# Performance work log

Hardware: AMD Instinct MI355X
Metric: run time of the kernel (lower is better)

Reference implementation:

```python
import jax, jax.numpy as jnp
import numpy as np

N_NODES = 100000
N_EDGES = 3200000
F_IN = 256
HIDDEN = 16
N_CLASSES = 32


def setup_inputs() -> dict:
    key = jax.random.key(0)
    ks = jax.random.split(key, 9)
    x = jax.random.normal(ks[0], (N_NODES, F_IN), dtype=jnp.float32)
    edge_index = jax.random.randint(ks[1], (2, N_EDGES), 0, N_NODES)
    edge_attr = jax.random.uniform(ks[2], (N_EDGES, 1), dtype=jnp.float32)
    s1 = 1.0 / np.sqrt(F_IN)
    W1 = jax.random.normal(ks[3], (2, F_IN, HIDDEN), dtype=jnp.float32) * s1
    root1 = jax.random.normal(ks[4], (F_IN, HIDDEN), dtype=jnp.float32) * s1
    bias1 = jnp.zeros((HIDDEN,), dtype=jnp.float32)
    s2 = 1.0 / np.sqrt(HIDDEN)
    W2 = jax.random.normal(ks[5], (2, HIDDEN, N_CLASSES), dtype=jnp.float32) * s2
    root2 = jax.random.normal(ks[6], (HIDDEN, N_CLASSES), dtype=jnp.float32) * s2
    bias2 = jnp.zeros((N_CLASSES,), dtype=jnp.float32)
    return {"x": x, "edge_attr": edge_attr, "W1": W1, "root1": root1,
            "bias1": bias1, "W2": W2, "root2": root2, "bias2": bias2,
            "edge_index": edge_index}


def spline_conv(x, src, dst, u, W, root, bias):
    """SplineConv, dim=1, kernel_size=2, degree=1, open spline, aggr='mean'.

    With K=2 and degree-1 open splines, v = u*(K-1) = u, so the B-spline basis
    per edge is simply ((1-u), u) over kernel weights W[0], W[1].
    """
    n = x.shape[0]
    # Node-level GEMMs once (cheaper than per-edge F_IN-dim gathers): [2, N, out]
    xs = jnp.einsum('nf,kfo->kno', x, W)
    # Per-edge basis-weighted message from source nodes: [E, out]
    msg = (1.0 - u)[:, None] * xs[0, src] + u[:, None] * xs[1, src]
    agg = jax.ops.segment_sum(msg, dst, num_segments=n)
    cnt = jax.ops.segment_sum(jnp.ones((dst.shape[0],), x.dtype), dst,
                              num_segments=n)
    return agg / jnp.maximum(cnt, 1.0)[:, None] + x @ root + bias


def reference(x, edge_attr, W1, root1, bias1, W2, root2, bias2, edge_index):
    src, dst = edge_index[0], edge_index[1]
    u = jnp.clip(edge_attr[:, 0], 0.0, 1.0)  # pseudo coords in [0, 1]
    # dropout with training=False is identity (eval-mode reference)
    h = jax.nn.elu(spline_conv(x, src, dst, u, W1, root1, bias1))
    out = spline_conv(h, src, dst, u, W2, root2, bias2)
    return jax.nn.log_softmax(out, axis=1)
```

## Files before the change

kernel.cpp:

```cpp
#include <hip/hip_runtime.h>
#include <hip/hip_fp16.h>
#include <math.h>

#define NN 100000
#define NE 3200000
#define FIN 256
#define HID 16
#define NC 32
#define NBUK 782
#define CAP 5120
#define SC_BLOCKS 250
#define SC_TILE 12800
#define SC_EPT 13
#define SK 20

typedef __attribute__((ext_vector_type(8))) short short8;
typedef __attribute__((ext_vector_type(4))) float f32x4;
typedef union { uint4 u; short8 s; } U8;

__global__ __launch_bounds__(256) void k_prepB(
    const float* __restrict__ W1, const float* __restrict__ root1,
    uint4* __restrict__ Bpk)
{
    int idx = blockIdx.x * 256 + threadIdx.x;
    if (idx >= 1536) return;
    int c = idx & 15, kc = (idx >> 4) & 31, t = idx >> 9;
    unsigned hi[8], lo[8];
    #pragma unroll
    for (int e = 0; e < 8; ++e) {
        int k = kc * 8 + e;
        float v;
        if (t == 0)      v = W1[k * 16 + c];
        else if (t == 1) v = W1[FIN * 16 + k * 16 + c];
        else             v = root1[k * 16 + c];
        unsigned u = __float_as_uint(v);
        unsigned h = u & 0xFFFF0000u;
        float lf = v - __uint_as_float(h);
        hi[e] = h;
        lo[e] = __float_as_uint(lf) & 0xFFFF0000u;
    }
    uint4 H, L;
    H.x = (hi[0] >> 16) | hi[1];  H.y = (hi[2] >> 16) | hi[3];
    H.z = (hi[4] >> 16) | hi[5];  H.w = (hi[6] >> 16) | hi[7];
    L.x = (lo[0] >> 16) | lo[1];  L.y = (lo[2] >> 16) | lo[3];
    L.z = (lo[4] >> 16) | lo[5];  L.w = (lo[6] >> 16) | lo[7];
    Bpk[(size_t)idx * 2]     = H;
    Bpk[(size_t)idx * 2 + 1] = L;
}

__global__ __launch_bounds__(256) void k_gemm1(
    const float* __restrict__ x, const uint4* __restrict__ Bpk,
    const float* __restrict__ bias1,
    __half2* __restrict__ xs1p, __half2* __restrict__ r1h)
{
    int wid = (blockIdx.x << 2) + (threadIdx.x >> 6);
    if (wid >= NN / 16) return;
    int lane = threadIdx.x & 63;
    int c = lane & 15, kcl = lane >> 4;
    int n0 = wid * 16;

    const float* xr = x + (size_t)(n0 + c) * FIN + kcl * 8;
    f32x4 acc0 = {0.f, 0.f, 0.f, 0.f};
    f32x4 acc1 = {0.f, 0.f, 0.f, 0.f};
    f32x4 acc2 = {0.f, 0.f, 0.f, 0.f};

    #define PACK(f0, f1, HO, LO) {                                     \
        unsigned u0 = __float_as_uint(f0), u1 = __float_as_uint(f1);   \
        unsigned h0 = u0 & 0xFFFF0000u, h1 = u1 & 0xFFFF0000u;         \
        HO = (h0 >> 16) | h1;                                          \
        float l0 = (f0) - __uint_as_float(h0);                         \
        float l1 = (f1) - __uint_as_float(h1);                         \
        LO = (__float_as_uint(l0) >> 16) |                             \
             (__float_as_uint(l1) & 0xFFFF0000u); }

    #pragma unroll
    for (int s = 0; s < 8; ++s) {
        float4 a0 = *(const float4*)(xr + s * 32);
        float4 a1 = *(const float4*)(xr + s * 32 + 4);
        U8 ahi, alo;
        PACK(a0.x, a0.y, ahi.u.x, alo.u.x)
        PACK(a0.z, a0.w, ahi.u.y, alo.u.y)
        PACK(a1.x, a1.y, ahi.u.z, alo.u.z)
        PACK(a1.z, a1.w, ahi.u.w, alo.u.w)

        const uint4* bp = Bpk + ((size_t)((s * 4 + kcl) * 16 + c)) * 2;
        U8 bh0, bl0, bh1, bl1, bh2, bl2;
        bh0.u = bp[0];     bl0.u = bp[1];
        bh1.u = bp[1024];  bl1.u = bp[1025];
        bh2.u = bp[2048];  bl2.u = bp[2049];

        acc0 = __builtin_amdgcn_mfma_f32_16x16x32_bf16(ahi.s, bh0.s, acc0, 0, 0, 0);
        acc0 = __builtin_amdgcn_mfma_f32_16x16x32_bf16(alo.s, bh0.s, acc0, 0, 0, 0);
        acc0 = __builtin_amdgcn_mfma_f32_16x16x32_bf16(ahi.s, bl0.s, acc0, 0, 0, 0);
        acc1 = __builtin_amdgcn_mfma_f32_16x16x32_bf16(ahi.s, bh1.s, acc1, 0, 0, 0);
        acc1 = __builtin_amdgcn_mfma_f32_16x16x32_bf16(alo.s, bh1.s, acc1, 0, 0, 0);
        acc1 = __builtin_amdgcn_mfma_f32_16x16x32_bf16(ahi.s, bl1.s, acc1, 0, 0, 0);
        acc2 = __builtin_amdgcn_mfma_f32_16x16x32_bf16(ahi.s, bh2.s, acc2, 0, 0, 0);
        acc2 = __builtin_amdgcn_mfma_f32_16x16x32_bf16(alo.s, bh2.s, acc2, 0, 0, 0);
        acc2 = __builtin_amdgcn_mfma_f32_16x16x32_bf16(ahi.s, bl2.s, acc2, 0, 0, 0);
    }
    #undef PACK

    #pragma unroll
    for (int r = 0; r < 4; ++r) {
        int n = n0 + kcl * 4 + r;
        xs1p[(size_t)n * 16 + c] = __floats2half2_rn(acc0[r], acc1[r]);
    }
    float b = bias1[c];
    #pragma unroll
    for (int r = 0; r < 4; ++r) {
        int n = n0 + kcl * 4 + r;
        float v = acc2[r] + b;
        float vo = __shfl_xor(v, 1, 64);
        if (!(c & 1))
            r1h[(size_t)n * 8 + (c >> 1)] = __floats2half2_rn(v, vo);
    }
}

__global__ __launch_bounds__(1024) void k_binscatter(
    const int* __restrict__ ei, const float* __restrict__ ea,
    int* __restrict__ gcnt, uint2* __restrict__ rec)
{
    __shared__ int h[NBUK];
    int t = threadIdx.x;
    if (t < NBUK) h[t] = 0;
    __syncthreads();
    int e0 = blockIdx.x * SC_TILE;
    int   dl[SC_EPT];
    int   sl[SC_EPT];
    float ul[SC_EPT];
    #pragma unroll
    for (int k = 0; k < SC_EPT; ++k) {
        int i = t + k * 1024;
        if (i < SC_TILE) {
            dl[k] = ei[NE + e0 + i];
            sl[k] = ei[e0 + i];
            ul[k] = ea[e0 + i];
            atomicAdd(&h[dl[k] >> 7], 1);
        }
    }
    __syncthreads();
    if (t < NBUK) {
        int c = h[t];
        if (c) h[t] = t * CAP + atomicAdd(&gcnt[t], c);
    }
    __syncthreads();
    #pragma unroll
    for (int k = 0; k < SC_EPT; ++k) {
        int i = t + k * 1024;
        if (i < SC_TILE) {
            float u = fminf(fmaxf(ul[k], 0.f), 1.f);
            int pos = atomicAdd(&h[dl[k] >> 7], 1);
            uint2 r;
            r.x = (unsigned)sl[k] | ((unsigned)(dl[k] & 127) << 17);
            r.y = __float_as_uint(u);
            rec[pos] = r;
        }
    }
}

__global__ __launch_bounds__(256) void k_sort(
    const int* __restrict__ gcnt, uint2* __restrict__ rec,
    int* __restrict__ rstart, int* __restrict__ rend)
{
    __shared__ int cnt[128], cur[128], ss[128];
    int t = threadIdx.x;
    if (t < 128) cnt[t] = 0;
    __syncthreads();
    int start = blockIdx.x * CAP, m = gcnt[blockIdx.x];
    uint2 r[SK];
    int nr = 0;
    for (int i = start + t; i < start + m; i += 256) {
        uint2 v = rec[i];
        if (nr < SK) r[nr++] = v;
        atomicAdd(&cnt[(v.x >> 17) & 127], 1);
    }
    __syncthreads();
    if (t < 128) ss[t] = cnt[t];
    __syncthreads();
    for (int off = 1; off < 128; off <<= 1) {
        int a = (t < 128 && t >= off) ? ss[t - off] : 0;
        __syncthreads();
        if (t < 128) ss[t] += a;
        __syncthreads();
    }
    if (t < 128) {
        int excl = ss[t] - cnt[t];
        cur[t] = excl;
        int n = blockIdx.x * 128 + t;
        if (n < NN) {
            rstart[n] = start + excl;
            rend[n]   = start + excl + cnt[t];
        }
    }
    __syncthreads();
    for (int k = 0; k < nr; ++k) {
        int dl = (int)(r[k].x >> 17) & 127;
        int p = atomicAdd(&cur[dl], 1);
        rec[start + p] = r[k];
    }
}

__global__ __launch_bounds__(256) void k_agg1g2(
    const int* __restrict__ rstart, const int* __restrict__ rend,
    const uint2* __restrict__ rec, const uint2* __restrict__ xs,
    const __half2* __restrict__ r1h, __half2* __restrict__ hh2)
{
    int t = threadIdx.x;
    int nl = t >> 3, j = t & 7;
    int n = blockIdx.x * 32 + nl;
    int s = rstart[n], e = rend[n];
    int d = e - s;
    float a0 = 0.f, a1 = 0.f;

    #define ACC1(q, g) {                                            \
        float u = __uint_as_float((q).y);                           \
        float2 f0 = __half22float2(*(const __half2*)&(g).x);        \
        float2 f1 = __half22float2(*(const __half2*)&(g).y);        \
        a0 += (1.f - u) * f0.x + u * f0.y;                          \
        a1 += (1.f - u) * f1.x + u * f1.y; }

    int k = s;
    for (; k + 8 <= e; k += 8) {
        uint2 q[8], g[8];
        #pragma unroll
        for (int z = 0; z < 8; ++z) q[z] = rec[k + z];
        #pragma unroll
        for (int z = 0; z < 8; ++z) g[z] = xs[(size_t)(q[z].x & 0x1FFFF) * 8 + j];
        #pragma unroll
        for (int z = 0; z < 8; ++z) { ACC1(q[z], g[z]) }
    }
    for (; k < e; ++k) {
        uint2 q = rec[k];
        uint2 g = xs[(size_t)(q.x & 0x1FFFF) * 8 + j];
        ACC1(q, g)
    }
    #undef ACC1

    float inv = 1.f / fmaxf((float)d, 1.f);
    float2 rr = __half22float2(r1h[(size_t)n * 8 + j]);
    float v0 = a0 * inv + rr.x;
    float v1 = a1 * inv + rr.y;
    v0 = v0 > 0.f ? v0 : expm1f(v0);
    v1 = v1 > 0.f ? v1 : expm1f(v1);
    hh2[(size_t)n * 8 + j] = __floats2half2_rn(v0, v1);
}

__global__ __launch_bounds__(256) void k_agg2(
    const int* __restrict__ rstart, const int* __restrict__ rend,
    const uint2* __restrict__ rec, const uint2* __restrict__ hh,
    const float* __restrict__ W2, const float* __restrict__ root2,
    const float* __restrict__ bias2, float* __restrict__ out)
{
    __shared__ float wsm[1568];
    __shared__ float ssm[64 * 33];
    __shared__ float hv[64 * 18];
    int t = threadIdx.x;
    for (int i = t; i < 1568; i += 256)
        wsm[i] = (i < 1024) ? W2[i] : (i < 1536 ? root2[i - 1024] : bias2[i - 1536]);

    int nl = t >> 2, j = t & 3;
    int n = blockIdx.x * 64 + nl;
    bool valid = n < NN;
    int s = 0, e = 0;
    if (valid) { s = rstart[n]; e = rend[n]; }
    float s0[4] = {0.f, 0.f, 0.f, 0.f};
    float s1[4] = {0.f, 0.f, 0.f, 0.f};

    #define ACC2(q, g) {                                            \
        float u = __uint_as_float((q).y);                           \
        float w0 = 1.f - u;                                         \
        float2 f0 = __half22float2(*(const __half2*)&(g).x);        \
        float2 f1 = __half22float2(*(const __half2*)&(g).y);        \
        s0[0] += w0 * f0.x; s1[0] += u * f0.x;                      \
        s0[1] += w0 * f0.y; s1[1] += u * f0.y;                      \
        s0[2] += w0 * f1.x; s1[2] += u * f1.x;                      \
        s0[3] += w0 * f1.y; s1[3] += u * f1.y; }

    int k = s;
    for (; k + 8 <= e; k += 8) {
        uint2 q[8], g[8];
        #pragma unroll
        for (int z = 0; z < 8; ++z) q[z] = rec[k + z];
        #pragma unroll
        for (int z = 0; z < 8; ++z) g[z] = hh[(size_t)(q[z].x & 0x1FFFF) * 4 + j];
        #pragma unroll
        for (int z = 0; z < 8; ++z) { ACC2(q[z], g[z]) }
    }
    for (; k < e; ++k) {
        uint2 q = rec[k];
        uint2 g = hh[(size_t)(q.x & 0x1FFFF) * 4 + j];
        ACC2(q, g)
    }
    #undef ACC2

    float inv = 1.f / fmaxf((float)(e - s), 1.f);
    #pragma unroll
    for (int q2 = 0; q2 < 4; ++q2) {
        ssm[nl * 33 + 4 * j + q2] = s0[q2];
        ssm[nl * 33 + 16 + 4 * j + q2] = s1[q2];
    }
    if (valid) {
        uint2 gh = hh[(size_t)n * 4 + j];
        float2 h0 = __half22float2(*(const __half2*)&gh.x);
        float2 h1 = __half22float2(*(const __half2*)&gh.y);
        hv[nl * 18 + 4 * j]     = h0.x;
        hv[nl * 18 + 4 * j + 1] = h0.y;
        hv[nl * 18 + 4 * j + 2] = h1.x;
        hv[nl * 18 + 4 * j + 3] = h1.y;
    } else {
        hv[nl * 18 + 4 * j]     = 0.f;
        hv[nl * 18 + 4 * j + 1] = 0.f;
        hv[nl * 18 + 4 * j + 2] = 0.f;
        hv[nl * 18 + 4 * j + 3] = 0.f;
    }
    if (j == 0) hv[nl * 18 + 16] = inv;
    __syncthreads();

    float invn = hv[nl * 18 + 16];
    float v[8];
    #pragma unroll
    for (int cc = 0; cc < 8; ++cc) {
        int c = j * 8 + cc;
        float acc = wsm[1536 + c];
        float agg = 0.f;
        #pragma unroll
        for (int kk = 0; kk < 16; ++kk) {
            agg += ssm[nl * 33 + kk] * wsm[kk * 32 + c]
                 + ssm[nl * 33 + 16 + kk] * wsm[512 + kk * 32 + c];
            acc += hv[nl * 18 + kk] * wsm[1024 + kk * 32 + c];
        }
        v[cc] = acc + agg * invn;
    }

    float m = v[0];
    #pragma unroll
    for (int cc = 1; cc < 8; ++cc) m = fmaxf(m, v[cc]);
    #pragma unroll
    for (int off = 1; off < 4; off <<= 1)
        m = fmaxf(m, __shfl_xor(m, off, 4));
    float sm = 0.f;
    #pragma unroll
    for (int cc = 0; cc < 8; ++cc) sm += expf(v[cc] - m);
    #pragma unroll
    for (int off = 1; off < 4; off <<= 1)
        sm += __shfl_xor(sm, off, 4);
    float ls = m + logf(sm);
    if (valid) {
        float4* op = (float4*)(out + (size_t)n * 32 + j * 8);
        op[0] = make_float4(v[0] - ls, v[1] - ls, v[2] - ls, v[3] - ls);
        op[1] = make_float4(v[4] - ls, v[5] - ls, v[6] - ls, v[7] - ls);
    }
}

extern "C" void kernel_launch(void* const* d_in, const int* in_sizes, int n_in,
                              void* d_out, int out_size, void* d_ws, size_t ws_size,
                              hipStream_t stream)
{
    const float* x     = (const float*)d_in[0];
    const float* ea    = (const float*)d_in[1];
    const float* W1    = (const float*)d_in[2];
    const float* root1 = (const float*)d_in[3];
    const float* bias1 = (const float*)d_in[4];
    const float* W2    = (const float*)d_in[5];
    const float* root2 = (const float*)d_in[6];
    const float* bias2 = (const float*)d_in[7];
    const int*   ei    = (const int*)d_in[8];
    float* out = (float*)d_out;

    float* ws = (float*)d_ws;
    __half2* xs1p = (__half2*)ws;
    __half2* r1h  = (__half2*)(ws + (size_t)NN * 16);
    __half2* hh2  = (__half2*)(ws + (size_t)NN * 24);
    uint2*   rec  = (uint2*)(ws + (size_t)NN * 32);
    int*     iws  = (int*)(ws + (size_t)NN * 32 + (size_t)NBUK * CAP * 2);
    int* rstart = iws;
    int* rend   = iws + NN;
    int* gcnt   = iws + 2 * NN;
    uint4* Bpk = (uint4*)(ws + (size_t)NN * 24);

    hipMemsetAsync(gcnt, 0, NBUK * sizeof(int), stream);

    k_prepB<<<6, 256, 0, stream>>>(W1, root1, Bpk);
    k_gemm1<<<(NN / 16 + 3) / 4, 256, 0, stream>>>(x, Bpk, bias1, xs1p, r1h);
    k_binscatter<<<SC_BLOCKS, 1024, 0, stream>>>(ei, ea, gcnt, rec);
    k_sort<<<NBUK, 256, 0, stream>>>(gcnt, rec, rstart, rend);
    k_agg1g2<<<(NN * 8) / 256, 256, 0, stream>>>(rstart, rend, rec,
                                                 (const uint2*)xs1p, r1h, hh2);
    k_agg2<<<(NN + 63) / 64, 256, 0, stream>>>(rstart, rend, rec,
                                               (const uint2*)hh2,
                                               W2, root2, bias2, out);
}
```

Baseline: 382.4 us.

## Replace per-bucket sort with shared-memory atomic aggregation per destination bucket

Removes the k_sort pass and the rstart/rend CSR arrays. Each block now walks one 128-node destination bucket's unsorted records and accumulates messages into shared-memory float accumulators with LDS atomics, counting degrees the same way. This saves a full read/write pass over the edge records and one kernel launch. In exchange it adds heavy LDS atomic contention, and the per-node dense tail in layer 2 (32 outputs by 16 features) now runs on only 128 of 512 threads.

Measured after the change: 1.292 ms. 3.38x slower.

```diff
diff --git a/kernel.cpp b/kernel.cpp
--- a/kernel.cpp
+++ b/kernel.cpp
@@ -12,7 +12,6 @@
 #define SC_BLOCKS 250
 #define SC_TILE 12800
 #define SC_EPT 13
-#define SK 20
 
 typedef __attribute__((ext_vector_type(8))) short short8;
 typedef __attribute__((ext_vector_type(4))) float f32x4;
@@ -159,197 +158,155 @@
     }
 }
 
-__global__ __launch_bounds__(256) void k_sort(
-    const int* __restrict__ gcnt, uint2* __restrict__ rec,
-    int* __restrict__ rstart, int* __restrict__ rend)
-{
-    __shared__ int cnt[128], cur[128], ss[128];
+__global__ __launch_bounds__(512) void k_agg1b(
+    const int* __restrict__ gcnt, const uint2* __restrict__ rec,
+    const uint2* __restrict__ xs, const __half2* __restrict__ r1h,
+    __half2* __restrict__ hh2)
+{
+    __shared__ float acc[128 * 17];
+    __shared__ int cnt[128];
     int t = threadIdx.x;
+    #pragma unroll
+    for (int i = t; i < 128 * 17; i += 512) acc[i] = 0.f;
     if (t < 128) cnt[t] = 0;
     __syncthreads();
-    int start = blockIdx.x * CAP, m = gcnt[blockIdx.x];
-    uint2 r[SK];
-    int nr = 0;
-    for (int i = start + t; i < start + m; i += 256) {
-        uint2 v = rec[i];
-        if (nr < SK) r[nr++] = v;
-        atomicAdd(&cnt[(v.x >> 17) & 127], 1);
-    }
-    __syncthreads();
-    if (t < 128) ss[t] = cnt[t];
-    __syncthreads();
-    for (int off = 1; off < 128; off <<= 1) {
-        int a = (t < 128 && t >= off) ? ss[t - off] : 0;
-        __syncthreads();
-        if (t < 128) ss[t] += a;
-        __syncthreads();
-    }
+
+    int b = blockIdx.x;
+    int base = b * CAP, m = gcnt[b];
+    int rl = t >> 3, j = t & 7;
+
+    #define DO1(q, g) {                                                 \
+        int dl_ = ((q).x >> 17) & 127;                                  \
+        float u_ = __uint_as_float((q).y);                              \
+        float2 f0 = __half22float2(*(const __half2*)&(g).x);            \
+        float2 f1 = __half22float2(*(const __half2*)&(g).y);            \
+        atomicAdd(&acc[dl_ * 17 + 2 * j],     (1.f - u_) * f0.x + u_ * f0.y); \
+        atomicAdd(&acc[dl_ * 17 + 2 * j + 1], (1.f - u_) * f1.x + u_ * f1.y); \
+        if (j == 0) atomicAdd(&cnt[dl_], 1); }
+
+    int k = rl;
+    for (; k + 256 <= m; k += 256) {
+        uint2 q[4], g[4];
+        #pragma unroll
+        for (int z = 0; z < 4; ++z) q[z] = rec[base + k + 64 * z];
+        #pragma unroll
+        for (int z = 0; z < 4; ++z) g[z] = xs[(size_t)(q[z].x & 0x1FFFF) * 8 + j];
+        #pragma unroll
+        for (int z = 0; z < 4; ++z) { DO1(q[z], g[z]) }
+    }
+    for (; k < m; k += 64) {
+        uint2 q = rec[base + k];
+        uint2 g = xs[(size_t)(q.x & 0x1FFFF) * 8 + j];
+        DO1(q, g)
+    }
+    #undef DO1
+    __syncthreads();
+
     if (t < 128) {
-        int excl = ss[t] - cnt[t];
-        cur[t] = excl;
-        int n = blockIdx.x * 128 + t;
+        int n = b * 128 + t;
         if (n < NN) {
-            rstart[n] = start + excl;
-            rend[n]   = start + excl + cnt[t];
+            float inv = 1.f / fmaxf((float)cnt[t], 1.f);
+            __half2* hp = hh2 + (size_t)n * 8;
+            const __half2* rp = r1h + (size_t)n * 8;
+            #pragma unroll
+            for (int w = 0; w < 8; ++w) {
+                float2 rr = __half22float2(rp[w]);
+                float v0 = acc[t * 17 + 2 * w] * inv + rr.x;
+                float v1 = acc[t * 17 + 2 * w + 1] * inv + rr.y;
+                v0 = v0 > 0.f ? v0 : expm1f(v0);
+                v1 = v1 > 0.f ? v1 : expm1f(v1);
+                hp[w] = __floats2half2_rn(v0, v1);
+            }
         }
     }
-    __syncthreads();
-    for (int k = 0; k < nr; ++k) {
-        int dl = (int)(r[k].x >> 17) & 127;
-        int p = atomicAdd(&cur[dl], 1);
-        rec[start + p] = r[k];
-    }
-}
-
-__global__ __launch_bounds__(256) void k_agg1g2(
-    const int* __restrict__ rstart, const int* __restrict__ rend,
-    const uint2* __restrict__ rec, const uint2* __restrict__ xs,
-    const __half2* __restrict__ r1h, __half2* __restrict__ hh2)
-{
+}
+
+__global__ __launch_bounds__(512) void k_agg2b(
+    const int* __restrict__ gcnt, const uint2* __restrict__ rec,
+    const __half2* __restrict__ hh, const float* __restrict__ W2,
+    const float* __restrict__ root2, const float* __restrict__ bias2,
+    float* __restrict__ out)
+{
+    __shared__ float wsm[1568];
+    __shared__ float acc[128 * 33];
+    __shared__ int cnt[128];
     int t = threadIdx.x;
-    int nl = t >> 3, j = t & 7;
-    int n = blockIdx.x * 32 + nl;
-    int s = rstart[n], e = rend[n];
-    int d = e - s;
-    float a0 = 0.f, a1 = 0.f;
-
-    #define ACC1(q, g) {                                            \
-        float u = __uint_as_float((q).y);                           \
-        float2 f0 = __half22float2(*(const __half2*)&(g).x);        \
-        float2 f1 = __half22float2(*(const __half2*)&(g).y);        \
-        a0 += (1.f - u) * f0.x + u * f0.y;                          \
-        a1 += (1.f - u) * f1.x + u * f1.y; }
-
-    int k = s;
-    for (; k + 8 <= e; k += 8) {
-        uint2 q[8], g[8];
-        #pragma unroll
-        for (int z = 0; z < 8; ++z) q[z] = rec[k + z];
-        #pragma unroll
-        for (int z = 0; z < 8; ++z) g[z] = xs[(size_t)(q[z].x & 0x1FFFF) * 8 + j];
-        #pragma unroll
-        for (int z = 0; z < 8; ++z) { ACC1(q[z], g[z]) }
-    }
-    for (; k < e; ++k) {
-        uint2 q = rec[k];
-        uint2 g = xs[(size_t)(q.x & 0x1FFFF) * 8 + j];
-        ACC1(q, g)
-    }
-    #undef ACC1
-
-    float inv = 1.f / fmaxf((float)d, 1.f);
-    float2 rr = __half22float2(r1h[(size_t)n * 8 + j]);
-    float v0 = a0 * inv + rr.x;
-    float v1 = a1 * inv + rr.y;
-    v0 = v0 > 0.f ? v0 : expm1f(v0);
-    v1 = v1 > 0.f ? v1 : expm1f(v1);
-    hh2[(size_t)n * 8 + j] = __floats2half2_rn(v0, v1);
-}
-
-__global__ __launch_bounds__(256) void k_agg2(
-    const int* __restrict__ rstart, const int* __restrict__ rend,
-    const uint2* __restrict__ rec, const uint2* __restrict__ hh,
-    const float* __restrict__ W2, const float* __restrict__ root2,
-    const float* __restrict__ bias2, float* __restrict__ out)
-{
-    __shared__ float wsm[1568];
-    __shared__ float ssm[64 * 33];
-    __shared__ float hv[64 * 18];
-    int t = threadIdx.x;
-    for (int i = t; i < 1568; i += 256)
+    for (int i = t; i < 1568; i += 512)
         wsm[i] = (i < 1024) ? W2[i] : (i < 1536 ? root2[i - 1024] : bias2[i - 1536]);
-
-    int nl = t >> 2, j = t & 3;
-    int n = blockIdx.x * 64 + nl;
-    bool valid = n < NN;
-    int s = 0, e = 0;
-    if (valid) { s = rstart[n]; e = rend[n]; }
-    float s0[4] = {0.f, 0.f, 0.f, 0.f};
-    float s1[4] = {0.f, 0.f, 0.f, 0.f};
-
-    #define ACC2(q, g) {                                            \
-        float u = __uint_as_float((q).y);                           \
-        float w0 = 1.f - u;                                         \
-        float2 f0 = __half22float2(*(const __half2*)&(g).x);        \
-        float2 f1 = __half22float2(*(const __half2*)&(g).y);        \
-        s0[0] += w0 * f0.x; s1[0] += u * f0.x;                      \
-        s0[1] += w0 * f0.y; s1[1] += u * f0.y;                      \
-        s0[2] += w0 * f1.x; s1[2] += u * f1.x;                      \
-        s0[3] += w0 * f1.y; s1[3] += u * f1.y; }
-
-    int k = s;
-    for (; k + 8 <= e; k += 8) {
-        uint2 q[8], g[8];
-        #pragma unroll
-        for (int z = 0; z < 8; ++z) q[z] = rec[k + z];
-        #pragma unroll
-        for (int z = 0; z < 8; ++z) g[z] = hh[(size_t)(q[z].x & 0x1FFFF) * 4 + j];
-        #pragma unroll
-        for (int z = 0; z < 8; ++z) { ACC2(q[z], g[z]) }
-    }
-    for (; k < e; ++k) {
-        uint2 q = rec[k];
-        uint2 g = hh[(size_t)(q.x & 0x1FFFF) * 4 + j];
-        ACC2(q, g)
-    }
-    #undef ACC2
-
-    float inv = 1.f / fmaxf((float)(e - s), 1.f);
-    #pragma unroll
-    for (int q2 = 0; q2 < 4; ++q2) {
-        ssm[nl * 33 + 4 * j + q2] = s0[q2];
-        ssm[nl * 33 + 16 + 4 * j + q2] = s1[q2];
-    }
-    if (valid) {
-        uint2 gh = hh[(size_t)n * 4 + j];
-        float2 h0 = __half22float2(*(const __half2*)&gh.x);
-        float2 h1 = __half22float2(*(const __half2*)&gh.y);
-        hv[nl * 18 + 4 * j]     = h0.x;
-        hv[nl * 18 + 4 * j + 1] = h0.y;
-        hv[nl * 18 + 4 * j + 2] = h1.x;
-        hv[nl * 18 + 4 * j + 3] = h1.y;
-    } else {
-        hv[nl * 18 + 4 * j]     = 0.f;
-        hv[nl * 18 + 4 * j + 1] = 0.f;
-        hv[nl * 18 + 4 * j + 2] = 0.f;
-        hv[nl * 18 + 4 * j + 3] = 0.f;
-    }
-    if (j == 0) hv[nl * 18 + 16] = inv;
-    __syncthreads();
-
-    float invn = hv[nl * 18 + 16];
-    float v[8];
-    #pragma unroll
-    for (int cc = 0; cc < 8; ++cc) {
-        int c = j * 8 + cc;
-        float acc = wsm[1536 + c];
-        float agg = 0.f;
-        #pragma unroll
-        for (int kk = 0; kk < 16; ++kk) {
-            agg += ssm[nl * 33 + kk] * wsm[kk * 32 + c]
-                 + ssm[nl * 33 + 16 + kk] * wsm[512 + kk * 32 + c];
-            acc += hv[nl * 18 + kk] * wsm[1024 + kk * 32 + c];
+    #pragma unroll
+    for (int i = t; i < 128 * 33; i += 512) acc[i] = 0.f;
+    if (t < 128) cnt[t] = 0;
+    __syncthreads();
+
+    int b = blockIdx.x;
+    int base = b * CAP, m = gcnt[b];
+    int rl = t >> 3, j = t & 7;
+
+    #define DO2(q, g) {                                                 \
+        int dl_ = ((q).x >> 17) & 127;                                  \
+        float u_ = __uint_as_float((q).y);                              \
+        float w0_ = 1.f - u_;                                           \
+        float2 f = __half22float2(g);                                   \
+        atomicAdd(&acc[dl_ * 33 + 2 * j],          w0_ * f.x);          \
+        atomicAdd(&acc[dl_ * 33 + 2 * j + 1],      w0_ * f.y);          \
+        atomicAdd(&acc[dl_ * 33 + 16 + 2 * j],     u_ * f.x);           \
+        atomicAdd(&acc[dl_ * 33 + 16 + 2 * j + 1], u_ * f.y);           \
+        if (j == 0) atomicAdd(&cnt[dl_], 1); }
+
+    int k = rl;
+    for (; k + 256 <= m; k += 256) {
+        uint2 q[4]; __half2 g[4];
+        #pragma unroll
+        for (int z = 0; z < 4; ++z) q[z] = rec[base + k + 64 * z];
+        #pragma unroll
+        for (int z = 0; z < 4; ++z) g[z] = hh[(size_t)(q[z].x & 0x1FFFF) * 8 + j];
+        #pragma unroll
+        for (int z = 0; z < 4; ++z) { DO2(q[z], g[z]) }
+    }
+    for (; k < m; k += 64) {
+        uint2 q = rec[base + k];
+        __half2 g = hh[(size_t)(q.x & 0x1FFFF) * 8 + j];
+        DO2(q, g)
+    }
+    #undef DO2
+    __syncthreads();
+
+    if (t < 128) {
+        int n = b * 128 + t;
+        if (n < NN) {
+            float inv = 1.f / fmaxf((float)cnt[t], 1.f);
+            float h[16];
+            const __half2* hp = hh + (size_t)n * 8;
+            #pragma unroll
+            for (int w = 0; w < 8; ++w) {
+                float2 a = __half22float2(hp[w]);
+                h[2 * w] = a.x; h[2 * w + 1] = a.y;
+            }
+            float v[32];
+            #pragma unroll
+            for (int c = 0; c < 32; ++c) {
+                float agg = 0.f, rt = wsm[1536 + c];
+                #pragma unroll
+                for (int kk = 0; kk < 16; ++kk) {
+                    agg += acc[t * 33 + kk] * wsm[kk * 32 + c]
+                         + acc[t * 33 + 16 + kk] * wsm[512 + kk * 32 + c];
+                    rt  += h[kk] * wsm[1024 + kk * 32 + c];
+                }
+                v[c] = rt + agg * inv;
+            }
+            float mx = v[0];
+            #pragma unroll
+            for (int c = 1; c < 32; ++c) mx = fmaxf(mx, v[c]);
+            float sm = 0.f;
+            #pragma unroll
+            for (int c = 0; c < 32; ++c) sm += expf(v[c] - mx);
+            float ls = mx + logf(sm);
+            float4* op = (float4*)(out + (size_t)n * 32);
+            #pragma unroll
+            for (int w = 0; w < 8; ++w)
+                op[w] = make_float4(v[4 * w] - ls, v[4 * w + 1] - ls,
+                                    v[4 * w + 2] - ls, v[4 * w + 3] - ls);
         }
-        v[cc] = acc + agg * invn;
-    }
-
-    float m = v[0];
-    #pragma unroll
-    for (int cc = 1; cc < 8; ++cc) m = fmaxf(m, v[cc]);
-    #pragma unroll
-    for (int off = 1; off < 4; off <<= 1)
-        m = fmaxf(m, __shfl_xor(m, off, 4));
-    float sm = 0.f;
-    #pragma unroll
-    for (int cc = 0; cc < 8; ++cc) sm += expf(v[cc] - m);
-    #pragma unroll
-    for (int off = 1; off < 4; off <<= 1)
-        sm += __shfl_xor(sm, off, 4);
-    float ls = m + logf(sm);
-    if (valid) {
-        float4* op = (float4*)(out + (size_t)n * 32 + j * 8);
-        op[0] = make_float4(v[0] - ls, v[1] - ls, v[2] - ls, v[3] - ls);
-        op[1] = make_float4(v[4] - ls, v[5] - ls, v[6] - ls, v[7] - ls);
     }
 }
 
@@ -373,10 +330,7 @@
     __half2* r1h  = (__half2*)(ws + (size_t)NN * 16);
     __half2* hh2  = (__half2*)(ws + (size_t)NN * 24);
     uint2*   rec  = (uint2*)(ws + (size_t)NN * 32);
-    int*     iws  = (int*)(ws + (size_t)NN * 32 + (size_t)NBUK * CAP * 2);
-    int* rstart = iws;
-    int* rend   = iws + NN;
-    int* gcnt   = iws + 2 * NN;
+    int*     gcnt = (int*)(ws + (size_t)NN * 32 + (size_t)NBUK * CAP * 2);
     uint4* Bpk = (uint4*)(ws + (size_t)NN * 24);
 
     hipMemsetAsync(gcnt, 0, NBUK * sizeof(int), stream);
@@ -384,10 +338,6 @@
     k_prepB<<<6, 256, 0, stream>>>(W1, root1, Bpk);
     k_gemm1<<<(NN / 16 + 3) / 4, 256, 0, stream>>>(x, Bpk, bias1, xs1p, r1h);
     k_binscatter<<<SC_BLOCKS, 1024, 0, stream>>>(ei, ea, gcnt, rec);
-    k_sort<<<NBUK, 256, 0, stream>>>(gcnt, rec, rstart, rend);
-    k_agg1g2<<<(NN * 8) / 256, 256, 0, stream>>>(rstart, rend, rec,
-                                                 (const uint2*)xs1p, r1h, hh2);
-    k_agg2<<<(NN + 63) / 64, 256, 0, stream>>>(rstart, rend, rec,
-                                               (const uint2*)hh2,
-                                               W2, root2, bias2, out);
-}
+    k_agg1b<<<NBUK, 512, 0, stream>>>(gcnt, rec, (const uint2*)xs1p, r1h, hh2);
+    k_agg2b<<<NBUK, 512, 0, stream>>>(gcnt, rec, hh2, W2, root2, bias2, out);
+}
```
